# Optimization experiments

Hardware: AMD Instinct MI355X
Metric: run time of the kernel (lower is better)

The kernel has to match this reference:

```python
import jax, jax.numpy as jnp
import numpy as np

N = 50000      # nodes
E = 800000     # edges
T_MAX = 128
N_T = 128
NF = T_MAX * 3 # 384 node features


def setup_inputs() -> dict:
    key = jax.random.key(0)
    ks = jax.random.split(key, 12)
    def lin(k, fi, fo):
        k1, k2 = jax.random.split(k)
        s = 1.0 / np.sqrt(fi)
        return (jax.random.uniform(k1, (fi, fo), jnp.float32, -s, s),
                jax.random.uniform(k2, (fo,), jnp.float32, -s, s))
    x = jax.random.normal(ks[0], (N, NF), jnp.float32)
    edge_index = jax.random.randint(ks[1], (2, E), 0, N, jnp.int32)
    W1, b1 = lin(ks[2], NF, N_T)
    W2, b2 = lin(ks[3], N_T, N_T * 3)
    W3, b3 = lin(ks[4], N_T * 3, N_T * 2)
    W4, b4 = lin(ks[5], N_T * 2, NF)
    Wl, bl = lin(ks[6], NF, T_MAX)
    return {"x": x, "edge_index": edge_index,
            "W1": W1, "b1": b1, "W2": W2, "b2": b2,
            "W3": W3, "b3": b3, "W4": W4, "b4": b4,
            "Wl": Wl, "bl": bl}


def reference(x, edge_index, W1, b1, W2, b2, W3, b3, W4, b4, Wl, bl):
    # GCNConv (PyG defaults): add self-loops, symmetric normalization
    loop = jnp.arange(N, dtype=edge_index.dtype)
    src = jnp.concatenate([edge_index[0], loop])
    dst = jnp.concatenate([edge_index[1], loop])
    deg = jax.ops.segment_sum(jnp.ones_like(src, jnp.float32), dst, num_segments=N)
    dinv = jax.lax.rsqrt(deg)  # deg >= 1 due to self-loops
    norm = (dinv[src] * dinv[dst])[:, None]  # [E+N, 1]

    def gcn(h, W, b):
        hw = h @ W                       # [N, out]
        msg = hw[src] * norm             # gather + scale per edge
        agg = jax.ops.segment_sum(msg, dst, num_segments=N)
        return agg + b

    # dropout is identity in eval mode
    h = jax.nn.leaky_relu(gcn(x, W1, b1))
    h = jax.nn.leaky_relu(gcn(h, W2, b2))
    h = jax.nn.leaky_relu(gcn(h, W3, b3))
    h = jax.nn.leaky_relu(gcn(h, W4, b4))
    h = h @ Wl + bl
    return jax.nn.relu(h)  # args.schedule_deviation == False
```

## Files before the change

### kernel.cpp

```cpp
#include <hip/hip_runtime.h>

#define NNODES 50000
#define NEDGES 800000
#define NTILES ((NNODES + 255) / 256)
#define XFEAT (NNODES * 384)
#define XPREP_BLOCKS (XFEAT / (256 * 8))
#define WPREP_TOTAL 344064
#define WPREP_BLOCKS (WPREP_TOTAL / 256)

typedef unsigned short ushort_t;
typedef __attribute__((ext_vector_type(8))) short short8;
typedef __attribute__((ext_vector_type(4))) float floatx4;

__device__ __forceinline__ float bf2f(unsigned short u) {
  union { unsigned int i; float f; } v; v.i = ((unsigned int)u) << 16; return v.f;
}
__device__ __forceinline__ unsigned short f2bf(float f) {
  union { float f; unsigned int i; } v; v.f = f;
  unsigned int r = v.i + 0x7fffu + ((v.i >> 16) & 1u);
  return (unsigned short)(r >> 16);
}

__device__ __forceinline__ void gload_lds16(const void* g, void* l) {
  __builtin_amdgcn_global_load_lds(
      (const __attribute__((address_space(1))) unsigned int*)g,
      (__attribute__((address_space(3))) unsigned int*)l, 16, 0, 0);
}


__global__ void hist_kernel(const int* dst, int* cnt) {
  int i = blockIdx.x * 256 + threadIdx.x;
  if (i < NEDGES) atomicAdd(&cnt[dst[i]], 1);
}


__global__ __launch_bounds__(256) void tile_scan_kernel(
    const int* __restrict__ cnt, int* __restrict__ tile_pref, int* __restrict__ tile_sum) {
  __shared__ int s[256];
  int b = blockIdx.x, t = threadIdx.x;
  int i = b * 256 + t;
  int v = (i < NNODES) ? cnt[i] : 0;
  s[t] = v;
  __syncthreads();
#pragma unroll
  for (int off = 1; off < 256; off <<= 1) {
    int x = (t >= off) ? s[t - off] : 0;
    __syncthreads();
    s[t] += x;
    __syncthreads();
  }
  if (i < NNODES) tile_pref[i] = s[t] - v;
  if (t == 255) tile_sum[b] = s[255];
}

__global__ __launch_bounds__(256) void sum_scan_kernel(
    const int* __restrict__ tile_sum, int* __restrict__ tile_base) {
  __shared__ int s[256];
  int t = threadIdx.x;
  int v = (t < NTILES) ? tile_sum[t] : 0;
  s[t] = v;
  __syncthreads();
#pragma unroll
  for (int off = 1; off < 256; off <<= 1) {
    int x = (t >= off) ? s[t - off] : 0;
    __syncthreads();
    s[t] += x;
    __syncthreads();
  }
  if (t < NTILES) tile_base[t] = s[t] - v;
}

__global__ __launch_bounds__(256) void scan_write_kernel(
    const int* __restrict__ cnt, const int* __restrict__ tile_pref,
    const int* __restrict__ tile_base, int* __restrict__ row_ptr,
    int* __restrict__ cursor, float* __restrict__ dinv) {
  int b = blockIdx.x, t = threadIdx.x;
  int i = b * 256 + t;
  if (i < NNODES) {
    int base = tile_base[b] + tile_pref[i];
    row_ptr[i] = base;
    cursor[i] = base;
    dinv[i] = rsqrtf((float)(cnt[i] + 1));
    if (i == NNODES - 1) row_ptr[NNODES] = base + cnt[i];
  }
}

__global__ void fill_kernel(const int* src, const int* dst, int* cursor, int* col_idx) {
  int i = blockIdx.x * 256 + threadIdx.x;
  if (i < NEDGES) {
    int p = atomicAdd(&cursor[dst[i]], 1);
    col_idx[p] = src[i];
  }
}

__global__ __launch_bounds__(256) void prep_all(
    const float* __restrict__ x, ushort_t* __restrict__ xbf,
    const float* __restrict__ W1, ushort_t* __restrict__ W1h, ushort_t* __restrict__ W1l,
    const float* __restrict__ W2, ushort_t* __restrict__ W2h, ushort_t* __restrict__ W2l,
    const float* __restrict__ W3, ushort_t* __restrict__ W3h, ushort_t* __restrict__ W3l,
    const float* __restrict__ W4, ushort_t* __restrict__ W4h, ushort_t* __restrict__ W4l,
    const float* __restrict__ Wl, ushort_t* __restrict__ Wlh, ushort_t* __restrict__ Wll) {
  int b = blockIdx.x;
  if (b < XPREP_BLOCKS) {
    size_t i = ((size_t)b * 256 + threadIdx.x) * 8;
    float4 p0 = *(const float4*)(x + i);
    float4 p1 = *(const float4*)(x + i + 4);
    uint4 u;
    u.x = (unsigned int)f2bf(p0.x) | ((unsigned int)f2bf(p0.y) << 16);
    u.y = (unsigned int)f2bf(p0.z) | ((unsigned int)f2bf(p0.w) << 16);
    u.z = (unsigned int)f2bf(p1.x) | ((unsigned int)f2bf(p1.y) << 16);
    u.w = (unsigned int)f2bf(p1.z) | ((unsigned int)f2bf(p1.w) << 16);
    *(uint4*)(xbf + i) = u;
    return;
  }
  int t = (b - XPREP_BLOCKS) * 256 + threadIdx.x;
  const float* W; ushort_t* hi; ushort_t* lo; int K, N;
  if (t < 49152)       { W = W1; hi = W1h; lo = W1l; K = 384; N = 128; }
  else if (t < 98304)  { W = W2; hi = W2h; lo = W2l; K = 128; N = 384; t -= 49152; }
  else if (t < 196608) { W = W3; hi = W3h; lo = W3l; K = 384; N = 256; t -= 98304; }
  else if (t < 294912) { W = W4; hi = W4h; lo = W4l; K = 256; N = 384; t -= 196608; }
  else                 { W = Wl; hi = Wlh; lo = Wll; K = 384; N = 128; t -= 294912; }
  int n = t / K, k = t - n * K;
  float w = W[(size_t)k * N + n];
  unsigned short h = f2bf(w);
  hi[t] = h;
  lo[t] = f2bf(w - bf2f(h));
}


template <int WH>
__device__ __forceinline__ void load_rowh(const ushort_t* p, float* f) {
  if (WH == 1) {
    f[0] = bf2f(*p);
  } else {
    unsigned int u = *(const unsigned int*)p;
    f[0] = bf2f((unsigned short)(u & 0xffff));
    f[1] = bf2f((unsigned short)(u >> 16));
  }
}

template <int C>
__global__ __launch_bounds__(256) void agg_kernel(
    const ushort_t* __restrict__ in, ushort_t* __restrict__ out,
    const int* __restrict__ row_ptr, const int* __restrict__ col_idx,
    const float* __restrict__ dinv, const float* __restrict__ bias,
    int mode, int scale_store) {
  constexpr int WH = C / 128;
  int b = blockIdx.x;
  int half = (b >> 2) & 1;
  int idx = (b >> 3) * 4 + (b & 3);
  if (idx >= 3125) return;
  int wave = idx * 4 + (int)(threadIdx.x >> 6);
  int lane = threadIdx.x & 63;
  int co = half * (C / 2) + lane * WH;
  const ushort_t* base = in + co;
  float bb[WH];
  if (mode) {
    if (WH == 1) {
      bb[0] = bias[co];
    } else {
      float2 b2 = *(const float2*)(bias + co);
      bb[0] = b2.x; bb[1] = b2.y;
    }
  }
  for (int k = 0; k < 4; ++k) {
    int wid = __builtin_amdgcn_readfirstlane(wave * 4 + k);
    float acc[WH];
    load_rowh<WH>(base + (size_t)wid * C, acc);
    int e = row_ptr[wid], e1 = row_ptr[wid + 1];
    for (; e + 16 <= e1; e += 16) {
      int j[16];
#pragma unroll
      for (int q = 0; q < 16; ++q) j[q] = col_idx[e + q];
      float v[16][WH];
#pragma unroll
      for (int q = 0; q < 16; ++q) load_rowh<WH>(base + (size_t)j[q] * C, v[q]);
#pragma unroll
      for (int c = 0; c < WH; ++c) {
        float s0 = (v[0][c] + v[1][c]) + (v[2][c] + v[3][c]);
        float s1 = (v[4][c] + v[5][c]) + (v[6][c] + v[7][c]);
        float s2 = (v[8][c] + v[9][c]) + (v[10][c] + v[11][c]);
        float s3 = (v[12][c] + v[13][c]) + (v[14][c] + v[15][c]);
        acc[c] += (s0 + s1) + (s2 + s3);
      }
    }
    for (; e + 4 <= e1; e += 4) {
      int j0 = col_idx[e], j1 = col_idx[e + 1], j2 = col_idx[e + 2], j3 = col_idx[e + 3];
      float v0[WH], v1[WH], v2[WH], v3[WH];
      load_rowh<WH>(base + (size_t)j0 * C, v0);
      load_rowh<WH>(base + (size_t)j1 * C, v1);
      load_rowh<WH>(base + (size_t)j2 * C, v2);
      load_rowh<WH>(base + (size_t)j3 * C, v3);
#pragma unroll
      for (int c = 0; c < WH; ++c) acc[c] += (v0[c] + v1[c]) + (v2[c] + v3[c]);
    }
    for (; e < e1; ++e) {
      int j = col_idx[e];
      float v[WH];
      load_rowh<WH>(base + (size_t)j * C, v);
#pragma unroll
      for (int c = 0; c < WH; ++c) acc[c] += v[c];
    }
    float di = dinv[wid];
    if (mode) {
      float sc = scale_store ? di : 1.f;
#pragma unroll
      for (int c = 0; c < WH; ++c) {
        float v = acc[c] * di + bb[c];
        v = v > 0.f ? v : 0.01f * v;
        acc[c] = v * sc;
      }
    } else {
#pragma unroll
      for (int c = 0; c < WH; ++c) acc[c] *= di;
    }
    if (WH == 1) {
      out[(size_t)wid * C + co] = f2bf(acc[0]);
    } else {
      *(unsigned int*)(out + (size_t)wid * C + co) =
          (unsigned int)f2bf(acc[0]) | ((unsigned int)f2bf(acc[1]) << 16);
    }
  }
}


#define BK 32

template <int TB>
__device__ __forceinline__ void stage_tile(const ushort_t* __restrict__ G, int g0,
                                           int K, int kb, ushort_t* lds,
                                           int tid, int w, int Mclamp) {
  constexpr int IT = TB / 64;
#pragma unroll
  for (int it = 0; it < IT; ++it) {
    int s = it * 256 + tid;
    int row = s >> 2;
    int j = (s & 3) ^ ((s >> 3) & 3);
    int gr = g0 + row; if (gr > Mclamp - 1) gr = Mclamp - 1;
    gload_lds16(G + (size_t)gr * K + kb + j * 8,
                lds + (size_t)(it * 256 + w * 64) * 8);
  }
}

template <int TBM, int TBN>
__global__ __launch_bounds__(256, TBM == 64 ? 6 : 3) void gemm_mfma(
    const ushort_t* __restrict__ A, const ushort_t* __restrict__ Bhi,
    const ushort_t* __restrict__ Blo, void* __restrict__ Cv,
    const float* __restrict__ bias, const float* __restrict__ dinv,
    int M, int K, int ldc, int mode, int scale_store, int out_f32) {
  constexpr int FR = TBM / 32;
  constexpr int FG = TBN / 32;
  __shared__ ushort_t As[2][TBM * BK];
  __shared__ ushort_t Bh[2][TBN * BK];
  __shared__ ushort_t Bl[2][TBN * BK];
  int tid = threadIdx.x;
  int lane = tid & 63, w = tid >> 6;
  int wm = w & 1, wn = w >> 1;

  int lin = blockIdx.y * gridDim.x + blockIdx.x;
  int nwg = gridDim.x * gridDim.y;
  int q = nwg >> 3, r = nwg & 7, xc = lin & 7, sdx = lin >> 3;
  int wg = (xc < r ? xc * (q + 1) : r * (q + 1) + (xc - r) * q) + sdx;
  int nty = gridDim.y;
  int tx = wg / nty, ty = wg - tx * nty;
  int m0 = tx * TBM, n0 = ty * TBN;

  floatx4 acc[FR][FG] = {};
  int nkt = K / BK;
  int cur = 0;
  stage_tile<TBM>(A, m0, K, 0, As[0], tid, w, M);
  stage_tile<TBN>(Bhi, n0, K, 0, Bh[0], tid, w, 1 << 30);
  stage_tile<TBN>(Blo, n0, K, 0, Bl[0], tid, w, 1 << 30);
  __syncthreads();
  int rr = lane & 15, jj = lane >> 4;
  for (int kt = 0; kt < nkt; ++kt) {
    if (kt + 1 < nkt) {
      int kb = (kt + 1) * BK;
      stage_tile<TBM>(A, m0, K, kb, As[cur ^ 1], tid, w, M);
      stage_tile<TBN>(Bhi, n0, K, kb, Bh[cur ^ 1], tid, w, 1 << 30);
      stage_tile<TBN>(Blo, n0, K, kb, Bl[cur ^ 1], tid, w, 1 << 30);
    }
    __builtin_amdgcn_sched_barrier(0);
    short8 af[FR], fh[FG], fl[FG];
#pragma unroll
    for (int f = 0; f < FR; ++f) {
      int fr_row = wm * (TBM / 2) + f * 16 + rr;
      af[f] = *(const short8*)&As[cur][fr_row * BK + ((jj ^ ((fr_row >> 1) & 3)) * 8)];
    }
#pragma unroll
    for (int g = 0; g < FG; ++g) {
      int fb_row = wn * (TBN / 2) + g * 16 + rr;
      int o = fb_row * BK + ((jj ^ ((fb_row >> 1) & 3)) * 8);
      fh[g] = *(const short8*)&Bh[cur][o];
      fl[g] = *(const short8*)&Bl[cur][o];
    }
#pragma unroll
    for (int f = 0; f < FR; ++f)
#pragma unroll
      for (int g = 0; g < FG; ++g) {
        acc[f][g] = __builtin_amdgcn_mfma_f32_16x16x32_bf16(af[f], fh[g], acc[f][g], 0, 0, 0);
        acc[f][g] = __builtin_amdgcn_mfma_f32_16x16x32_bf16(af[f], fl[g], acc[f][g], 0, 0, 0);
      }
    __syncthreads();
    cur ^= 1;
  }
  int cr = lane >> 4, cc = lane & 15;
#pragma unroll
  for (int f = 0; f < FR; ++f) {
#pragma unroll
    for (int r2 = 0; r2 < 4; ++r2) {
      int row = m0 + wm * (TBM / 2) + f * 16 + cr * 4 + r2;
      if (row >= M) continue;
      float sc = scale_store ? dinv[row] : 1.f;
#pragma unroll
      for (int g = 0; g < FG; ++g) {
        int col = n0 + wn * (TBN / 2) + g * 16 + cc;
        float v = acc[f][g][r2];
        if (mode) {
          v += bias[col];
          v = (mode == 1) ? (v > 0.f ? v : 0.01f * v) : (v > 0.f ? v : 0.f);
        }
        v *= sc;
        if (out_f32) ((float*)Cv)[(size_t)row * ldc + col] = v;
        else ((ushort_t*)Cv)[(size_t)row * ldc + col] = f2bf(v);
      }
    }
  }
}


extern "C" void kernel_launch(void* const* d_in, const int* in_sizes, int n_in,
                              void* d_out, int out_size, void* d_ws, size_t ws_size,
                              hipStream_t stream) {
  const float* x  = (const float*)d_in[0];
  const int* ei   = (const int*)d_in[1];
  const float* W1 = (const float*)d_in[2];
  const float* b1 = (const float*)d_in[3];
  const float* W2 = (const float*)d_in[4];
  const float* b2 = (const float*)d_in[5];
  const float* W3 = (const float*)d_in[6];
  const float* b3 = (const float*)d_in[7];
  const float* W4 = (const float*)d_in[8];
  const float* b4 = (const float*)d_in[9];
  const float* Wl = (const float*)d_in[10];
  const float* bl = (const float*)d_in[11];

  char* p = (char*)d_ws;
  auto alloc = [&](size_t bytes) {
    char* r = p;
    p += (bytes + 255) & ~(size_t)255;
    return r;
  };
  int* cnt       = (int*)alloc((size_t)NNODES * 4);
  int* cursor    = (int*)alloc((size_t)NNODES * 4);
  int* row_ptr   = (int*)alloc((size_t)(NNODES + 1) * 4);
  float* dinv    = (float*)alloc((size_t)NNODES * 4);
  int* col_idx   = (int*)alloc((size_t)NEDGES * 4);
  int* tile_pref = (int*)alloc((size_t)NNODES * 4);
  int* tile_sum  = (int*)alloc(256 * 4);
  int* tile_base = (int*)alloc(256 * 4);
  ushort_t* W1h = (ushort_t*)alloc(49152 * 2); ushort_t* W1l = (ushort_t*)alloc(49152 * 2);
  ushort_t* W2h = (ushort_t*)alloc(49152 * 2); ushort_t* W2l = (ushort_t*)alloc(49152 * 2);
  ushort_t* W3h = (ushort_t*)alloc(98304 * 2); ushort_t* W3l = (ushort_t*)alloc(98304 * 2);
  ushort_t* W4h = (ushort_t*)alloc(98304 * 2); ushort_t* W4l = (ushort_t*)alloc(98304 * 2);
  ushort_t* Wlh = (ushort_t*)alloc(49152 * 2); ushort_t* Wll = (ushort_t*)alloc(49152 * 2);
  ushort_t* actA = (ushort_t*)alloc((size_t)NNODES * 384 * 2);
  ushort_t* actB = (ushort_t*)alloc((size_t)NNODES * 384 * 2);
  ushort_t* xbf = actB;

  const int* src = ei;
  const int* dst = ei + NEDGES;

  hipMemsetAsync(cnt, 0, (size_t)NNODES * 4, stream);
  hist_kernel<<<(NEDGES + 255) / 256, 256, 0, stream>>>(dst, cnt);
  tile_scan_kernel<<<NTILES, 256, 0, stream>>>(cnt, tile_pref, tile_sum);
  sum_scan_kernel<<<1, 256, 0, stream>>>(tile_sum, tile_base);
  scan_write_kernel<<<NTILES, 256, 0, stream>>>(cnt, tile_pref, tile_base, row_ptr, cursor, dinv);
  fill_kernel<<<(NEDGES + 255) / 256, 256, 0, stream>>>(src, dst, cursor, col_idx);

  prep_all<<<XPREP_BLOCKS + WPREP_BLOCKS, 256, 0, stream>>>(
      x, xbf, W1, W1h, W1l, W2, W2h, W2l, W3, W3h, W3l, W4, W4h, W4l, Wl, Wlh, Wll);

  dim3 blk(256);
  int gm64  = (NNODES + 63) / 64;
  int gm128 = (NNODES + 127) / 128;
  int gagg  = 6256;

  gemm_mfma<64, 64><<<dim3(gm64, 2), blk, 0, stream>>>(xbf, W1h, W1l, actA, (const float*)0, dinv, NNODES, 384, 128, 0, 1, 0);
  agg_kernel<128><<<gagg, blk, 0, stream>>>(actA, actB, row_ptr, col_idx, dinv, b1, 1, 1);
  agg_kernel<128><<<gagg, blk, 0, stream>>>(actB, actA, row_ptr, col_idx, dinv, (const float*)0, 0, 0);
  gemm_mfma<128, 128><<<dim3(gm128, 3), blk, 0, stream>>>(actA, W2h, W2l, actB, b2, dinv, NNODES, 128, 384, 1, 0, 0);
  gemm_mfma<128, 128><<<dim3(gm128, 2), blk, 0, stream>>>(actB, W3h, W3l, actA, (const float*)0, dinv, NNODES, 384, 256, 0, 1, 0);
  agg_kernel<256><<<gagg, blk, 0, stream>>>(actA, actB, row_ptr, col_idx, dinv, b3, 1, 1);
  agg_kernel<256><<<gagg, blk, 0, stream>>>(actB, actA, row_ptr, col_idx, dinv, (const float*)0, 0, 0);
  gemm_mfma<128, 128><<<dim3(gm128, 3), blk, 0, stream>>>(actA, W4h, W4l, actB, b4, dinv, NNODES, 256, 384, 1, 0, 0);
  gemm_mfma<64, 64><<<dim3(gm64, 2), blk, 0, stream>>>(actB, Wlh, Wll, d_out, bl, dinv, NNODES, 384, 128, 2, 0, 1);
}
```

Before: 597.0 us.

## Partition histogram and CSR fill atomics by destination-node slice

The histogram and CSR fill kernels now launch 8 blocks per edge chunk, and each block handles only the edges whose destination falls in one eighth of the node range. The intent is for consecutive blocks to keep their atomics inside a smaller node range, so the atomic traffic hits fewer cache lines and L2 channels at a time and contention drops. In exchange, every edge index is read 8 times and most threads run the bounds check without doing an atomic.

```diff
diff --git a/kernel.cpp b/kernel.cpp
--- a/kernel.cpp
+++ b/kernel.cpp
@@ -7,6 +7,9 @@
 #define XPREP_BLOCKS (XFEAT / (256 * 8))
 #define WPREP_TOTAL 344064
 #define WPREP_BLOCKS (WPREP_TOTAL / 256)
+#define NODES_PER_SLICE (NNODES / 8)
+#define EDGES_PER_BLOCK 2048
+#define EDGE_BLOCKS ((NEDGES + EDGES_PER_BLOCK - 1) / EDGES_PER_BLOCK)
 
 typedef unsigned short ushort_t;
 typedef __attribute__((ext_vector_type(8))) short short8;
@@ -28,9 +31,40 @@
 }
 
 
-__global__ void hist_kernel(const int* dst, int* cnt) {
-  int i = blockIdx.x * 256 + threadIdx.x;
-  if (i < NEDGES) atomicAdd(&cnt[dst[i]], 1);
+__global__ __launch_bounds__(256) void hist_kernel(const int* __restrict__ dst,
+                                                   int* __restrict__ cnt) {
+  int b = blockIdx.x;
+  int lo = (b & 7) * NODES_PER_SLICE, hi = lo + NODES_PER_SLICE;
+  int base = (b >> 3) * EDGES_PER_BLOCK + threadIdx.x;
+#pragma unroll
+  for (int q = 0; q < EDGES_PER_BLOCK / 256; ++q) {
+    int i = base + q * 256;
+    if (i < NEDGES) {
+      int d = dst[i];
+      if (d >= lo && d < hi) atomicAdd(&cnt[d], 1);
+    }
+  }
+}
+
+__global__ __launch_bounds__(256) void fill_kernel(const int* __restrict__ src,
+                                                   const int* __restrict__ dst,
+                                                   int* __restrict__ cursor,
+                                                   int* __restrict__ col_idx) {
+  int b = blockIdx.x;
+  int lo = (b & 7) * NODES_PER_SLICE, hi = lo + NODES_PER_SLICE;
+  int base = (b >> 3) * EDGES_PER_BLOCK + threadIdx.x;
+#pragma unroll
+  for (int q = 0; q < EDGES_PER_BLOCK / 256; ++q) {
+    int i = base + q * 256;
+    if (i < NEDGES) {
+      int d = dst[i];
+      int s = src[i];
+      if (d >= lo && d < hi) {
+        int p = atomicAdd(&cursor[d], 1);
+        col_idx[p] = s;
+      }
+    }
+  }
 }
 
 
@@ -82,14 +116,6 @@
     cursor[i] = base;
     dinv[i] = rsqrtf((float)(cnt[i] + 1));
     if (i == NNODES - 1) row_ptr[NNODES] = base + cnt[i];
-  }
-}
-
-__global__ void fill_kernel(const int* src, const int* dst, int* cursor, int* col_idx) {
-  int i = blockIdx.x * 256 + threadIdx.x;
-  if (i < NEDGES) {
-    int p = atomicAdd(&cursor[dst[i]], 1);
-    col_idx[p] = src[i];
   }
 }
 
@@ -372,11 +398,11 @@
   const int* dst = ei + NEDGES;
 
   hipMemsetAsync(cnt, 0, (size_t)NNODES * 4, stream);
-  hist_kernel<<<(NEDGES + 255) / 256, 256, 0, stream>>>(dst, cnt);
+  hist_kernel<<<EDGE_BLOCKS * 8, 256, 0, stream>>>(dst, cnt);
   tile_scan_kernel<<<NTILES, 256, 0, stream>>>(cnt, tile_pref, tile_sum);
   sum_scan_kernel<<<1, 256, 0, stream>>>(tile_sum, tile_base);
   scan_write_kernel<<<NTILES, 256, 0, stream>>>(cnt, tile_pref, tile_base, row_ptr, cursor, dinv);
-  fill_kernel<<<(NEDGES + 255) / 256, 256, 0, stream>>>(src, dst, cursor, col_idx);
+  fill_kernel<<<EDGE_BLOCKS * 8, 256, 0, stream>>>(src, dst, cursor, col_idx);
 
   prep_all<<<XPREP_BLOCKS + WPREP_BLOCKS, 256, 0, stream>>>(
       x, xbf, W1, W1h, W1l, W2, W2h, W2l, W3, W3h, W3l, W4, W4h, W4l, Wl, Wlh, Wll);
```

Result: no change. 589.2 us (-1.3%).
